# Performance work log

Measured on AMD Instinct MI355X. Metric: run time of the kernel, lower is better.

Reference implementation:

```python
import jax, jax.numpy as jnp
import numpy as np

NL = 4      # num_layers
DM = 1024   # hidden_size (d_model)
DI = 2048   # d_inner = expand * d_model
DS = 16     # d_state
DC = 4      # d_conv
DTR = 64    # dt_rank = ceil(d_model/16)
IN = 256    # input_size
OUT = 128   # output_size
B = 4096    # batch


def setup_inputs() -> dict:
    key = jax.random.key(0)
    ks = jax.random.split(key, 10)
    s = 0.02
    d = {}
    d['x'] = jax.random.normal(ks[0], (B, IN), dtype=jnp.float32)
    d['inp_w'] = jax.random.normal(ks[1], (DM, IN), dtype=jnp.float32) * s
    d['inp_b'] = jnp.zeros((DM,), jnp.float32)
    d['in_proj_w'] = jax.random.normal(ks[2], (NL, 2 * DI, DM), dtype=jnp.float32) * s
    d['conv_w'] = jax.random.normal(ks[3], (NL, DI, DC), dtype=jnp.float32) * s
    d['conv_b'] = jnp.zeros((NL, DI), jnp.float32)
    d['xproj_w'] = jax.random.normal(ks[4], (NL, DTR + 2 * DS, DI), dtype=jnp.float32) * s
    d['dt_w'] = jax.random.normal(ks[5], (NL, DI, DTR), dtype=jnp.float32) * s
    dt_init = jax.random.uniform(ks[6], (NL, DI), minval=1e-3, maxval=1e-1)
    d['dt_b'] = jnp.log(jnp.expm1(dt_init))  # softplus^-1 of target dt
    d['A_log'] = jnp.log(jnp.broadcast_to(jnp.arange(1, DS + 1, dtype=jnp.float32), (NL, DI, DS)))
    d['D_param'] = jnp.ones((NL, DI), jnp.float32)
    d['out_w'] = jax.random.normal(ks[7], (NL, DM, DI), dtype=jnp.float32) * s
    d['ln_g'] = jnp.ones((NL, DM), jnp.float32)
    d['ln_b'] = jnp.zeros((NL, DM), jnp.float32)
    d['outp_w'] = jax.random.normal(ks[8], (OUT, DM), dtype=jnp.float32) * s
    d['outp_b'] = jnp.zeros((OUT,), jnp.float32)
    return d


def _silu(x):
    return x * jax.nn.sigmoid(x)


def _layer_norm(x, g, b, eps=1e-5):
    mu = jnp.mean(x, axis=-1, keepdims=True)
    var = jnp.mean(jnp.square(x - mu), axis=-1, keepdims=True)
    return (x - mu) * jax.lax.rsqrt(var + eps) * g + b


def _mamba_block(x, in_w, cw, cb, xp_w, dtw, dtb, A_log, Dp, ow):
    # x: [B, L, DM]
    Bn, Ls, _ = x.shape
    xz = jnp.einsum('bld,ed->ble', x, in_w)              # [B,L,2*DI]
    xc, z = jnp.split(xz, 2, axis=-1)
    # causal depthwise conv1d (kernel DC, groups=DI)
    xpad = jnp.pad(xc, ((0, 0), (DC - 1, 0), (0, 0)))
    conv = cb + sum(xpad[:, k:k + Ls, :] * cw[:, k] for k in range(DC))
    xc = _silu(conv)
    x_dbl = jnp.einsum('bld,ed->ble', xc, xp_w)           # [B,L,DTR+2*DS]
    dt, Bm, Cm = jnp.split(x_dbl, [DTR, DTR + DS], axis=-1)
    dt = jax.nn.softplus(jnp.einsum('blr,dr->bld', dt, dtw) + dtb)  # [B,L,DI]
    A = -jnp.exp(A_log)                                   # [DI,DS]

    def step(h, inp):
        dt_t, B_t, C_t, x_t = inp                         # [B,DI],[B,DS],[B,DS],[B,DI]
        h = jnp.exp(dt_t[..., None] * A) * h + dt_t[..., None] * B_t[:, None, :] * x_t[..., None]
        y = jnp.einsum('bdn,bn->bd', h, C_t)
        return h, y

    h0 = jnp.zeros((Bn, DI, DS), dtype=x.dtype)
    xs = (jnp.moveaxis(dt, 1, 0), jnp.moveaxis(Bm, 1, 0), jnp.moveaxis(Cm, 1, 0), jnp.moveaxis(xc, 1, 0))
    _, ys = jax.lax.scan(step, h0, xs)
    y = jnp.moveaxis(ys, 0, 1) + Dp * xc                  # [B,L,DI]
    y = y * _silu(z)
    return jnp.einsum('bld,md->blm', y, ow)               # [B,L,DM]


def reference(x, inp_w, inp_b, in_proj_w, conv_w, conv_b, xproj_w, dt_w, dt_b,
              A_log, D_param, out_w, ln_g, ln_b, outp_w, outp_b):
    h = x[:, None, :]                                     # unsqueeze(1): [B,1,IN]
    h = jnp.einsum('bli,di->bld', h, inp_w) + inp_b       # input_proj
    for i in range(NL):
        res = h
        y = _mamba_block(h, in_proj_w[i], conv_w[i], conv_b[i], xproj_w[i],
                         dt_w[i], dt_b[i], A_log[i], D_param[i], out_w[i])
        y = _layer_norm(y, ln_g[i], ln_b[i])
        h = res + y                                       # dropout is identity in eval
    h = h[:, 0, :]                                        # squeeze(1)
    return jnp.einsum('bd,od->bo', h, outp_w) + outp_b
```

## Files before the change

### kernel.cpp

```cpp
#include <hip/hip_runtime.h>
#include <hip/hip_bf16.h>
#include <hip/hip_fp16.h>

#define NL 4
#define DM 1024
#define DI 2048
#define DS_N 16
#define DC 4
#define DTR 64
#define IN_DIM 256
#define OUT_DIM 128
#define BATCH 4096

typedef _Float16 half8 __attribute__((ext_vector_type(8)));
typedef _Float16 half4 __attribute__((ext_vector_type(4)));
typedef float floatx4 __attribute__((ext_vector_type(4)));

#define E_X      0L
#define E_INPW   (E_X + (long)BATCH * IN_DIM)
#define E_INPROJ (E_INPW + (long)DM * IN_DIM)
#define E_XPROJ  (E_INPROJ + (long)NL * 2 * DI * DM)
#define E_DTW    (E_XPROJ + (long)NL * (DTR + 2 * DS_N) * DI)
#define E_OUTW   (E_DTW + (long)NL * DI * DTR)
#define E_OUTPW  (E_OUTW + (long)NL * DM * DI)
#define E_TOT    (E_OUTPW + (long)OUT_DIM * DM)

__device__ __forceinline__ float silu_f(float x) {
    return x / (1.0f + __expf(-x));
}

__device__ __forceinline__ void gload_lds16(const _Float16* g, const _Float16* l) {
    __builtin_amdgcn_global_load_lds(
        (const __attribute__((address_space(1))) void*)(uintptr_t)g,
        (__attribute__((address_space(3))) void*)(uintptr_t)l,
        16, 0, 0);
}

__global__ __launch_bounds__(256) void cvt_k(
    const float* __restrict__ x, const float* __restrict__ inp_w,
    const float* __restrict__ in_proj_w, const float* __restrict__ xproj_w,
    const float* __restrict__ dt_w, const float* __restrict__ out_w,
    const float* __restrict__ outp_w, _Float16* __restrict__ dst)
{
    long i = ((long)blockIdx.x * 256 + threadIdx.x) * 8;
    const float* s;
    if      (i < E_INPW)   s = x         + (i - E_X);
    else if (i < E_INPROJ) s = inp_w     + (i - E_INPW);
    else if (i < E_XPROJ)  s = in_proj_w + (i - E_INPROJ);
    else if (i < E_DTW)    s = xproj_w   + (i - E_XPROJ);
    else if (i < E_OUTW)   s = dt_w      + (i - E_DTW);
    else if (i < E_OUTPW)  s = out_w     + (i - E_OUTW);
    else                   s = outp_w    + (i - E_OUTPW);
    float4 a = *(const float4*)s;
    float4 b = *(const float4*)(s + 4);
    half8 h;
    h[0]=(_Float16)a.x; h[1]=(_Float16)a.y; h[2]=(_Float16)a.z; h[3]=(_Float16)a.w;
    h[4]=(_Float16)b.x; h[5]=(_Float16)b.y; h[6]=(_Float16)b.z; h[7]=(_Float16)b.w;
    *(half8*)(dst + i) = h;
}

struct EpiP {
    float* o32;
    _Float16* o16;
    _Float16* o16b;
    const float* bias;
    const float* cw;
    const float* cb;
    const float* dtb;
    const float* Dp;
    const _Float16* xc;
    const _Float16* zs;
};

template<int EPI>
__global__ __launch_bounds__(256) void gemm_k(
    const _Float16* __restrict__ A, const _Float16* __restrict__ W,
    int N, int K, int lda, int kChunk, EpiP ep)
{
    __shared__ __align__(16) char smem[36864];
    _Float16* As = (_Float16*)smem;
    _Float16* Bs = (_Float16*)(smem + 8192);
    const int tid  = threadIdx.x;
    const int lane = tid & 63;
    const int wave = tid >> 6;
    const int wm = (wave >> 1) * 64;
    const int wn = (wave & 1) * 64;
    const int lr = lane & 15;
    const int lq = lane >> 4;
    const long tm = (long)blockIdx.y * 128;
    const int  tn = blockIdx.x * 128;

    const int p0 = wave * 128 + lane;
    const int r0 = p0 >> 2, c0 = ((p0 & 3) - ((r0 >> 1) & 3)) & 3;
    const int p1 = p0 + 64;
    const int r1 = p1 >> 2, c1 = ((p1 & 3) - ((r1 >> 1) & 3)) & 3;
    const _Float16* lA0 = &As[wave * 1024];
    const _Float16* lA1 = &As[wave * 1024 + 512];
    const _Float16* lB0 = &Bs[wave * 1024];
    const _Float16* lB1 = &Bs[wave * 1024 + 512];

    const int kBeg = blockIdx.z * kChunk;
    const _Float16* a0 = A + (tm + r0) * (long)lda + kBeg + c0 * 8;
    const _Float16* a1 = A + (tm + r1) * (long)lda + kBeg + c1 * 8;
    const _Float16* w0 = W + (long)min(tn + r0, N - 1) * K + kBeg + c0 * 8;
    const _Float16* w1 = W + (long)min(tn + r1, N - 1) * K + kBeg + c1 * 8;

    floatx4 acc[4][4];
#pragma unroll
    for (int i = 0; i < 4; i++)
#pragma unroll
        for (int j = 0; j < 4; j++) acc[i][j] = (floatx4)0.0f;

    for (int it = 0; it < kChunk / 32; it++) {
        gload_lds16(a0, lA0);
        gload_lds16(a1, lA1);
        gload_lds16(w0, lB0);
        gload_lds16(w1, lB1);
        a0 += 32; a1 += 32; w0 += 32; w1 += 32;
        __syncthreads();

        half8 af[4], bf[4];
#pragma unroll
        for (int i = 0; i < 4; i++) {
            int row = wm + i * 16 + lr;
            int slot = row * 4 + ((lq + (row >> 1)) & 3);
            af[i] = *(const half8*)&As[slot * 8];
        }
#pragma unroll
        for (int j = 0; j < 4; j++) {
            int row = wn + j * 16 + lr;
            int slot = row * 4 + ((lq + (row >> 1)) & 3);
            bf[j] = *(const half8*)&Bs[slot * 8];
        }
#pragma unroll
        for (int i = 0; i < 4; i++)
#pragma unroll
            for (int j = 0; j < 4; j++)
                acc[i][j] = __builtin_amdgcn_mfma_f32_16x16x32_f16(af[i], bf[j], acc[i][j], 0, 0, 0);
        __syncthreads();
    }

    if constexpr (EPI != 5) {
        _Float16* slab = (_Float16*)(smem + wave * 9216);
#pragma unroll
        for (int i = 0; i < 4; i++)
#pragma unroll
            for (int j = 0; j < 4; j++)
#pragma unroll
                for (int p = 0; p < 4; p++)
                    slab[(i * 16 + lq * 4 + p) * 72 + j * 16 + lr] = (_Float16)acc[i][j][p];

        const int rsub = lane >> 3;
        const int cch  = lane & 7;
        const int cb0  = tn + wn;
        const int n0   = cb0 + cch * 8;
        const long g0  = tm + wm;

        float bv[8], cwv[8], dtbv[8], dpv[8];
        if constexpr (EPI == 0) {
            float4 q0 = *(const float4*)&ep.bias[n0];
            float4 q1 = *(const float4*)&ep.bias[n0 + 4];
            bv[0]=q0.x; bv[1]=q0.y; bv[2]=q0.z; bv[3]=q0.w;
            bv[4]=q1.x; bv[5]=q1.y; bv[6]=q1.z; bv[7]=q1.w;
        }
        if constexpr (EPI == 1) {
            if (cb0 < DI) {
#pragma unroll
                for (int k = 0; k < 8; k++) cwv[k] = ep.cw[(n0 + k) * DC + 3];
                float4 q0 = *(const float4*)&ep.cb[n0];
                float4 q1 = *(const float4*)&ep.cb[n0 + 4];
                bv[0]=q0.x; bv[1]=q0.y; bv[2]=q0.z; bv[3]=q0.w;
                bv[4]=q1.x; bv[5]=q1.y; bv[6]=q1.z; bv[7]=q1.w;
            }
        }
        float bcv;
        if constexpr (EPI == 3) {
            float4 q0 = *(const float4*)&ep.dtb[n0];
            float4 q1 = *(const float4*)&ep.dtb[n0 + 4];
            dtbv[0]=q0.x; dtbv[1]=q0.y; dtbv[2]=q0.z; dtbv[3]=q0.w;
            dtbv[4]=q1.x; dtbv[5]=q1.y; dtbv[6]=q1.z; dtbv[7]=q1.w;
            float4 p0v = *(const float4*)&ep.Dp[n0];
            float4 p1v = *(const float4*)&ep.Dp[n0 + 4];
            dpv[0]=p0v.x; dpv[1]=p0v.y; dpv[2]=p0v.z; dpv[3]=p0v.w;
            dpv[4]=p1v.x; dpv[5]=p1v.y; dpv[6]=p1v.z; dpv[7]=p1v.w;
            const half8* pp = (const half8*)(A + (g0 + lane) * 96 + DTR);
            half8 b0 = pp[0], b1 = pp[1], c0v = pp[2], c1v = pp[3];
            float s = 0.0f;
#pragma unroll
            for (int k = 0; k < 8; k++)
                s += (float)b0[k] * (float)c0v[k] + (float)b1[k] * (float)c1v[k];
            bcv = s;
        }

#pragma unroll
        for (int r = 0; r < 8; r++) {
            long g = g0 + r * 8 + rsub;
            half8 hv = *(const half8*)&slab[(r * 8 + rsub) * 72 + cch * 8];
            if constexpr (EPI == 0) {
                float4 f0, f1; half8 o;
#pragma unroll
                for (int k = 0; k < 4; k++) {
                    float v = (float)hv[k] + bv[k];
                    (&f0.x)[k] = v; o[k] = (_Float16)v;
                }
#pragma unroll
                for (int k = 0; k < 4; k++) {
                    float v = (float)hv[k + 4] + bv[k + 4];
                    (&f1.x)[k] = v; o[k + 4] = (_Float16)v;
                }
                *(float4*)&ep.o32[g * DM + n0]     = f0;
                *(float4*)&ep.o32[g * DM + n0 + 4] = f1;
                *(half8*)&ep.o16[g * DM + n0] = o;
            } else if constexpr (EPI == 1) {
                half8 o;
                if (cb0 < DI) {
#pragma unroll
                    for (int k = 0; k < 8; k++) {
                        float s = (float)hv[k] * cwv[k] + bv[k];
                        o[k] = (_Float16)silu_f(s);
                    }
                    *(half8*)&ep.o16[g * DI + n0] = o;
                } else {
#pragma unroll
                    for (int k = 0; k < 8; k++) o[k] = (_Float16)silu_f((float)hv[k]);
                    *(half8*)&ep.o16b[g * DI + (n0 - DI)] = o;
                }
            } else if constexpr (EPI == 3) {
                float bc = __shfl(bcv, r * 8 + rsub, 64);
                half8 xcv = *(const half8*)&ep.xc[g * DI + n0];
                half8 zsv = *(const half8*)&ep.zs[g * DI + n0];
                half8 o;
#pragma unroll
                for (int k = 0; k < 8; k++) {
                    float dtv = (float)hv[k] + dtbv[k];
                    dtv = (dtv > 20.0f) ? dtv : log1pf(__expf(dtv));
                    float y = (float)xcv[k] * (dtv * bc + dpv[k]) * (float)zsv[k];
                    o[k] = (_Float16)y;
                }
                *(half8*)&ep.o16[g * DI + n0] = o;
            } else if constexpr (EPI == 4) {
                *(half8*)&ep.o16[g * DM + n0] = hv;
            } else {
                if (n0 < 96)
                    *(half8*)&ep.o16[((long)blockIdx.z * BATCH + g) * 96 + n0] = hv;
            }
        }
    } else {
#pragma unroll
        for (int i = 0; i < 4; i++) {
#pragma unroll
            for (int p = 0; p < 4; p++) {
                long m = tm + wm + i * 16 + lq * 4 + p;
#pragma unroll
                for (int j = 0; j < 4; j++) {
                    int n = tn + wn + j * 16 + lr;
                    if (n >= N) continue;
                    ep.o32[m * OUT_DIM + n] = acc[i][j][p] + ep.bias[n];
                }
            }
        }
    }
}

__global__ __launch_bounds__(256) void xred_k(
    const _Float16* __restrict__ part, _Float16* __restrict__ xdbl)
{
    long i = ((long)blockIdx.x * 256 + threadIdx.x) * 4;
    float s0 = 0.f, s1 = 0.f, s2 = 0.f, s3 = 0.f;
#pragma unroll
    for (int z = 0; z < 8; z++) {
        half4 v = *(const half4*)&part[(long)z * BATCH * 96 + i];
        s0 += (float)v[0]; s1 += (float)v[1]; s2 += (float)v[2]; s3 += (float)v[3];
    }
    half4 h;
    h[0] = (_Float16)s0; h[1] = (_Float16)s1; h[2] = (_Float16)s2; h[3] = (_Float16)s3;
    *(half4*)&xdbl[i] = h;
}

__global__ __launch_bounds__(256) void ln_k(
    const _Float16* __restrict__ xin, const float* __restrict__ g, const float* __restrict__ b,
    float* __restrict__ h32, _Float16* __restrict__ h16)
{
    long row = blockIdx.x;
    const _Float16* x = xin + row * DM;
    int t = threadIdx.x;
    float v[4];
    float s = 0.0f, ss = 0.0f;
#pragma unroll
    for (int i = 0; i < 4; i++) {
        v[i] = (float)x[t + i * 256];
        s += v[i];
        ss += v[i] * v[i];
    }
#pragma unroll
    for (int o = 32; o > 0; o >>= 1) {
        s  += __shfl_down(s, o, 64);
        ss += __shfl_down(ss, o, 64);
    }
    __shared__ float rs[4], rss[4];
    int wv = t >> 6, ln = t & 63;
    if (ln == 0) { rs[wv] = s; rss[wv] = ss; }
    __syncthreads();
    if (t == 0) {
        float S  = rs[0] + rs[1] + rs[2] + rs[3];
        float SS = rss[0] + rss[1] + rss[2] + rss[3];
        float mu = S / (float)DM;
        float var = SS / (float)DM - mu * mu;
        rs[0]  = mu;
        rss[0] = rsqrtf(var + 1e-5f);
    }
    __syncthreads();
    float mu = rs[0], rstd = rss[0];
#pragma unroll
    for (int i = 0; i < 4; i++) {
        int c = t + i * 256;
        float hv = h32[row * DM + c] + (v[i] - mu) * rstd * g[c] + b[c];
        h32[row * DM + c] = hv;
        h16[row * DM + c] = (_Float16)hv;
    }
}

extern "C" void kernel_launch(void* const* d_in, const int* in_sizes, int n_in,
                              void* d_out, int out_size, void* d_ws, size_t ws_size,
                              hipStream_t stream) {
    const float* x         = (const float*)d_in[0];
    const float* inp_w     = (const float*)d_in[1];
    const float* inp_b     = (const float*)d_in[2];
    const float* in_proj_w = (const float*)d_in[3];
    const float* conv_w    = (const float*)d_in[4];
    const float* conv_b    = (const float*)d_in[5];
    const float* xproj_w   = (const float*)d_in[6];
    const float* dt_w      = (const float*)d_in[7];
    const float* dt_b      = (const float*)d_in[8];
    const float* D_param   = (const float*)d_in[10];
    const float* out_w     = (const float*)d_in[11];
    const float* ln_g      = (const float*)d_in[12];
    const float* ln_b      = (const float*)d_in[13];
    const float* outp_w    = (const float*)d_in[14];
    const float* outp_b    = (const float*)d_in[15];

    char* ws = (char*)d_ws;
    _Float16* wf    = (_Float16*)ws;
    float*    h32   = (float*)   (ws + (56u  << 20));
    _Float16* h16   = (_Float16*)(ws + (72u  << 20));
    _Float16* xc16  = (_Float16*)(ws + (80u  << 20));
    _Float16* zs16  = (_Float16*)(ws + (96u  << 20));
    _Float16* lnin16= (_Float16*)(ws + (96u  << 20));
    _Float16* xdbl  = (_Float16*)(ws + (112u << 20));
    _Float16* xpart = (_Float16*)(ws + (114u << 20));

    dim3 blk(256);
    EpiP ep;

    cvt_k<<<dim3((unsigned)(E_TOT / (256 * 8))), blk, 0, stream>>>(
        x, inp_w, in_proj_w, xproj_w, dt_w, out_w, outp_w, wf);

    ep = EpiP{}; ep.bias = inp_b; ep.o32 = h32; ep.o16 = h16;
    gemm_k<0><<<dim3(DM / 128, BATCH / 128, 1), blk, 0, stream>>>(
        wf + E_X, wf + E_INPW, DM, IN_DIM, IN_DIM, IN_DIM, ep);

    for (int l = 0; l < NL; l++) {
        ep = EpiP{}; ep.o16 = xc16; ep.o16b = zs16;
        ep.cw = conv_w + (size_t)l * DI * DC; ep.cb = conv_b + (size_t)l * DI;
        gemm_k<1><<<dim3(2 * DI / 128, BATCH / 128, 1), blk, 0, stream>>>(
            h16, wf + E_INPROJ + (size_t)l * 2 * DI * DM, 2 * DI, DM, DM, DM, ep);

        ep = EpiP{}; ep.o16 = xpart;
        gemm_k<6><<<dim3(1, BATCH / 128, 8), blk, 0, stream>>>(
            xc16, wf + E_XPROJ + (size_t)l * (DTR + 2 * DS_N) * DI,
            DTR + 2 * DS_N, DI, DI, DI / 8, ep);

        xred_k<<<dim3(BATCH * 96 / 4 / 256), blk, 0, stream>>>(xpart, xdbl);

        ep = EpiP{}; ep.o16 = xc16;
        ep.dtb = dt_b + (size_t)l * DI; ep.Dp = D_param + (size_t)l * DI;
        ep.xc = xc16; ep.zs = zs16;
        gemm_k<3><<<dim3(DI / 128, BATCH / 128, 1), blk, 0, stream>>>(
            xdbl, wf + E_DTW + (size_t)l * DI * DTR, DI, DTR, 96, DTR, ep);

        ep = EpiP{}; ep.o16 = lnin16;
        gemm_k<4><<<dim3(DM / 128, BATCH / 128, 1), blk, 0, stream>>>(
            xc16, wf + E_OUTW + (size_t)l * DM * DI, DM, DI, DI, DI, ep);

        ln_k<<<dim3(BATCH), blk, 0, stream>>>(
            lnin16, ln_g + (size_t)l * DM, ln_b + (size_t)l * DM, h32, h16);
    }

    ep = EpiP{}; ep.bias = outp_b; ep.o32 = (float*)d_out;
    gemm_k<5><<<dim3(1, BATCH / 128, 1), blk, 0, stream>>>(
        h16, wf + E_OUTPW, OUT_DIM, DM, DM, DM, ep);
}
```

Baseline: 865.8 us.

## Double-buffer GEMM LDS tiles and split-K the out-projection into layernorm

The GEMM main loop now alternates between two LDS buffers. The next K-tile's global-to-LDS load is issued before the current tile's MFMAs, which removes one barrier per iteration and overlaps memory with compute. The out-projection GEMM is launched with two K-splits, so it runs twice as many blocks on a grid that was only 256 blocks. The two partial results are written to separate slabs and summed inside the layernorm kernel. This adds extra fp16 partial traffic and assumes the layernorm input buffer is large enough for two slabs.

```diff
diff --git a/kernel.cpp b/kernel.cpp
--- a/kernel.cpp
+++ b/kernel.cpp
@@ -78,8 +78,6 @@
     int N, int K, int lda, int kChunk, EpiP ep)
 {
     __shared__ __align__(16) char smem[36864];
-    _Float16* As = (_Float16*)smem;
-    _Float16* Bs = (_Float16*)(smem + 8192);
     const int tid  = threadIdx.x;
     const int lane = tid & 63;
     const int wave = tid >> 6;
@@ -94,10 +92,6 @@
     const int r0 = p0 >> 2, c0 = ((p0 & 3) - ((r0 >> 1) & 3)) & 3;
     const int p1 = p0 + 64;
     const int r1 = p1 >> 2, c1 = ((p1 & 3) - ((r1 >> 1) & 3)) & 3;
-    const _Float16* lA0 = &As[wave * 1024];
-    const _Float16* lA1 = &As[wave * 1024 + 512];
-    const _Float16* lB0 = &Bs[wave * 1024];
-    const _Float16* lB1 = &Bs[wave * 1024 + 512];
 
     const int kBeg = blockIdx.z * kChunk;
     const _Float16* a0 = A + (tm + r0) * (long)lda + kBeg + c0 * 8;
@@ -111,13 +105,23 @@
 #pragma unroll
         for (int j = 0; j < 4; j++) acc[i][j] = (floatx4)0.0f;
 
-    for (int it = 0; it < kChunk / 32; it++) {
-        gload_lds16(a0, lA0);
-        gload_lds16(a1, lA1);
-        gload_lds16(w0, lB0);
-        gload_lds16(w1, lB1);
+    const int iters = kChunk / 32;
+    auto stage = [&](int b) {
+        _Float16* As = (_Float16*)(smem + b * 16384);
+        _Float16* Bs = (_Float16*)(smem + b * 16384 + 8192);
+        gload_lds16(a0, &As[wave * 1024]);
+        gload_lds16(a1, &As[wave * 1024 + 512]);
+        gload_lds16(w0, &Bs[wave * 1024]);
+        gload_lds16(w1, &Bs[wave * 1024 + 512]);
         a0 += 32; a1 += 32; w0 += 32; w1 += 32;
+    };
+
+    stage(0);
+    for (int it = 0; it < iters; it++) {
         __syncthreads();
+        if (it + 1 < iters) stage((it + 1) & 1);
+        const _Float16* As = (const _Float16*)(smem + (it & 1) * 16384);
+        const _Float16* Bs = As + 4096;
 
         half8 af[4], bf[4];
 #pragma unroll
@@ -137,8 +141,8 @@
 #pragma unroll
             for (int j = 0; j < 4; j++)
                 acc[i][j] = __builtin_amdgcn_mfma_f32_16x16x32_f16(af[i], bf[j], acc[i][j], 0, 0, 0);
-        __syncthreads();
-    }
+    }
+    __syncthreads();
 
     if constexpr (EPI != 5) {
         _Float16* slab = (_Float16*)(smem + wave * 9216);
@@ -239,7 +243,7 @@
                 }
                 *(half8*)&ep.o16[g * DI + n0] = o;
             } else if constexpr (EPI == 4) {
-                *(half8*)&ep.o16[g * DM + n0] = hv;
+                *(half8*)&ep.o16[((long)blockIdx.z * BATCH + g) * DM + n0] = hv;
             } else {
                 if (n0 < 96)
                     *(half8*)&ep.o16[((long)blockIdx.z * BATCH + g) * 96 + n0] = hv;
@@ -282,13 +286,15 @@
     float* __restrict__ h32, _Float16* __restrict__ h16)
 {
     long row = blockIdx.x;
-    const _Float16* x = xin + row * DM;
+    const _Float16* x0 = xin + row * DM;
+    const _Float16* x1 = xin + ((long)BATCH + row) * DM;
     int t = threadIdx.x;
     float v[4];
     float s = 0.0f, ss = 0.0f;
 #pragma unroll
     for (int i = 0; i < 4; i++) {
-        v[i] = (float)x[t + i * 256];
+        int c = t + i * 256;
+        v[i] = (float)x0[c] + (float)x1[c];
         s += v[i];
         ss += v[i] * v[i];
     }
@@ -379,8 +385,8 @@
             xdbl, wf + E_DTW + (size_t)l * DI * DTR, DI, DTR, 96, DTR, ep);
 
         ep = EpiP{}; ep.o16 = lnin16;
-        gemm_k<4><<<dim3(DM / 128, BATCH / 128, 1), blk, 0, stream>>>(
-            xc16, wf + E_OUTW + (size_t)l * DM * DI, DM, DI, DI, DI, ep);
+        gemm_k<4><<<dim3(DM / 128, BATCH / 128, 2), blk, 0, stream>>>(
+            xc16, wf + E_OUTW + (size_t)l * DM * DI, DM, DI, DI, DI / 2, ep);
 
         ln_k<<<dim3(BATCH), blk, 0, stream>>>(
             lnin16, ln_g + (size_t)l * DM, ln_b + (size_t)l * DM, h32, h16);
```

New measurement: 727.4 us. 1.19x faster.
